# Optimization experiments

Hardware: AMD Instinct MI355X
Metric: run time of the kernel (lower is better)

The kernel has to match this reference:

```python
import jax, jax.numpy as jnp
import numpy as np

ALPHA = 1.0  # self.a buffer (alpha=1.0 default)


def setup_inputs() -> dict:
    key = jax.random.key(0)
    k1, k2, k3 = jax.random.split(key, 3)
    B, S, DIN, DOUT = 4, 2048, 4096, 4096
    # activations and weights are int8 in [-127, 127)
    x = jax.random.randint(k1, (B, S, DIN), -127, 127, dtype=jnp.int8)
    weight = jax.random.randint(k2, (DOUT, DIN), -127, 127, dtype=jnp.int8)
    bias = jax.random.normal(k3, (1, DOUT), dtype=jnp.float32)
    return {"x": x, "weight": weight, "bias": bias}


def reference(x, weight, bias):
    # x: [B, S, DIN] int8; weight: [DOUT, DIN] int8; bias: [1, DOUT] fp32
    x_shape = x.shape
    x2 = x.reshape(-1, x_shape[-1])  # [B*S, DIN]
    y = jnp.matmul(x2, weight.T, preferred_element_type=jnp.int32)  # [B*S, DOUT] int32
    # epilogue: y + round(bias / alpha); int32 + fp32 promotes to fp32 (matches torch)
    y = y.astype(jnp.float32) + jnp.round(bias / ALPHA)
    return y.reshape(*x_shape[:-1], y.shape[-1])
```

## Files before the change

### kernel.cpp

```cpp
#include <hip/hip_runtime.h>
#include <stdint.h>
#include <math.h>


typedef int i32x4 __attribute__((ext_vector_type(4)));
typedef int i32x16 __attribute__((ext_vector_type(16)));

static constexpr int Mdim = 8192;
static constexpr int Ndim = 4096;
static constexpr int Kdim = 4096;
static constexpr int BM = 128;
static constexpr int BN = 128;
static constexpr int BKb = 64;
static constexpr int NKT = Kdim / BKb;
static constexpr int BUF_BYTES = 16384;

typedef const __attribute__((address_space(1))) unsigned int gu32;
typedef __attribute__((address_space(3))) unsigned int lu32;

__device__ __forceinline__ void gload_lds16(const int8_t* g, char* l) {
    __builtin_amdgcn_global_load_lds((gu32*)g, (lu32*)l, 16, 0, 0);
}

__global__ void pack_i32_to_i8(const int* __restrict__ in,
                               unsigned int* __restrict__ out, int n4) {
    int idx = blockIdx.x * blockDim.x + threadIdx.x;
    int stride = gridDim.x * blockDim.x;
    for (int i = idx; i < n4; i += stride) {
        i32x4 v = ((const i32x4*)in)[i];
        unsigned int o = ((unsigned)v[0] & 0xffu)
                       | (((unsigned)v[1] & 0xffu) << 8)
                       | (((unsigned)v[2] & 0xffu) << 16)
                       | (((unsigned)v[3]) << 24);
        out[i] = o;
    }
}

__global__ __launch_bounds__(256, 2) void w8a8_gemm_kernel(
    const int8_t* __restrict__ X, const int8_t* __restrict__ Wt,
    const float* __restrict__ bias, float* __restrict__ out)
{
    __shared__ char smem[2 * BUF_BYTES];

    const int tid   = threadIdx.x;
    const int w     = tid >> 6;
    const int l     = tid & 63;
    const int lrow  = l & 31;
    const int khalf = l >> 5;
    const int wr    = w >> 1;
    const int wc    = w & 1;

    const int bm = blockIdx.x * BM;
    const int bn = blockIdx.y * BN;

    const int8_t* gA0 = X  + (long)(bm +      l) * Kdim + w * 16;
    const int8_t* gA1 = X  + (long)(bm + 64 + l) * Kdim + w * 16;
    const int8_t* gB0 = Wt + (long)(bn +      l) * Kdim + w * 16;
    const int8_t* gB1 = Wt + (long)(bn + 64 + l) * Kdim + w * 16;
    const int lA0 = (w * 128 +      l) * 16;
    const int lA1 = (w * 128 + 64 + l) * 16;
    const int lB0 = 8192 + (w * 128 +      l) * 16;
    const int lB1 = 8192 + (w * 128 + 64 + l) * 16;

    const int aRowOff = (wr * 64 + lrow) * 16;
    const int bRowOff = (wc * 64 + lrow) * 16;

    i32x16 acc[2][2] = {};

    gload_lds16(gA0, &smem[lA0]);
    gload_lds16(gA1, &smem[lA1]);
    gload_lds16(gB0, &smem[lB0]);
    gload_lds16(gB1, &smem[lB1]);
    asm volatile("s_waitcnt vmcnt(0)" ::: "memory");
    __syncthreads();

    int buf = 0;
    for (int kt = 0; kt < NKT; ++kt) {
        if (kt + 1 < NKT) {
            const int kb = (kt + 1) * BKb;
            const int nb = (buf ^ 1) * BUF_BYTES;
            gload_lds16(gA0 + kb, &smem[nb + lA0]);
            gload_lds16(gA1 + kb, &smem[nb + lA1]);
            gload_lds16(gB0 + kb, &smem[nb + lB0]);
            gload_lds16(gB1 + kb, &smem[nb + lB1]);
        }

        const char* sb = &smem[buf * BUF_BYTES];
        i32x4 af[2][2], bf[2][2];
#pragma unroll
        for (int ks = 0; ks < 2; ++ks) {
            const int slot = (ks * 2 + khalf) * 2048;
            af[0][ks] = *(const i32x4*)(sb + slot + aRowOff);
            af[1][ks] = *(const i32x4*)(sb + slot + aRowOff + 32 * 16);
            bf[0][ks] = *(const i32x4*)(sb + 8192 + slot + bRowOff);
            bf[1][ks] = *(const i32x4*)(sb + 8192 + slot + bRowOff + 32 * 16);
        }

#pragma unroll
        for (int ks = 0; ks < 2; ++ks)
#pragma unroll
            for (int mi = 0; mi < 2; ++mi)
#pragma unroll
                for (int ni = 0; ni < 2; ++ni)
                    acc[mi][ni] = __builtin_amdgcn_mfma_i32_32x32x32_i8(
                        af[mi][ks], bf[ni][ks], acc[mi][ni], 0, 0, 0);

        asm volatile("s_waitcnt vmcnt(0)" ::: "memory");
        __syncthreads();
        buf ^= 1;
    }

#pragma unroll
    for (int ni = 0; ni < 2; ++ni) {
        const int col = bn + wc * 64 + ni * 32 + lrow;
        const float badd = rintf(bias[col]);
#pragma unroll
        for (int mi = 0; mi < 2; ++mi) {
            const int rbase = bm + wr * 64 + mi * 32 + 4 * khalf;
#pragma unroll
            for (int r = 0; r < 16; ++r) {
                const int row = rbase + (r & 3) + 8 * (r >> 2);
                out[(long)row * Ndim + col] = (float)acc[mi][ni][r] + badd;
            }
        }
    }
}

extern "C" void kernel_launch(void* const* d_in, const int* in_sizes, int n_in,
                              void* d_out, int out_size, void* d_ws, size_t ws_size,
                              hipStream_t stream) {
    const int*   X32  = (const int*)d_in[0];
    const int*   W32  = (const int*)d_in[1];
    const float* bias = (const float*)d_in[2];
    float* out = (float*)d_out;

    int8_t* Xp = (int8_t*)d_ws;
    int8_t* Wp = (int8_t*)d_ws + (size_t)Mdim * Kdim;

    const int nX4 = Mdim * Kdim / 4;
    const int nW4 = Ndim * Kdim / 4;
    pack_i32_to_i8<<<2048, 256, 0, stream>>>(X32, (unsigned int*)Xp, nX4);
    pack_i32_to_i8<<<2048, 256, 0, stream>>>(W32, (unsigned int*)Wp, nW4);

    dim3 grid(Mdim / BM, Ndim / BN);
    w8a8_gemm_kernel<<<grid, dim3(256), 0, stream>>>(Xp, Wp, bias, out);
}
```

Before: 507.1 us.

## Switch to 256x256 tiles with 8-wave interleaved load/MFMA pipeline

Replaces the 128x128x64 four-wave GEMM with a 256x256x128 eight-wave kernel using 16x16x64 int8 MFMAs. Global-to-LDS loads for the next tiles are split into quarters and interleaved between four MFMA phases, with barriers and priority raising to overlap memory and compute. This is meant to raise arithmetic intensity and hide load latency, at the cost of much larger LDS use (one block per CU), more registers, and possible LDS bank conflicts.

```diff
diff --git a/kernel.cpp b/kernel.cpp
--- a/kernel.cpp
+++ b/kernel.cpp
@@ -4,16 +4,15 @@
 
 
 typedef int i32x4 __attribute__((ext_vector_type(4)));
-typedef int i32x16 __attribute__((ext_vector_type(16)));
 
 static constexpr int Mdim = 8192;
 static constexpr int Ndim = 4096;
 static constexpr int Kdim = 4096;
-static constexpr int BM = 128;
-static constexpr int BN = 128;
-static constexpr int BKb = 64;
+static constexpr int BM = 256;
+static constexpr int BN = 256;
+static constexpr int BKb = 128;
 static constexpr int NKT = Kdim / BKb;
-static constexpr int BUF_BYTES = 16384;
+static constexpr int BUF_BYTES = 65536;
 
 typedef const __attribute__((address_space(1))) unsigned int gu32;
 typedef __attribute__((address_space(3))) unsigned int lu32;
@@ -36,92 +35,159 @@
     }
 }
 
-__global__ __launch_bounds__(256, 2) void w8a8_gemm_kernel(
+__global__ __launch_bounds__(512, 2) void w8a8_gemm_256(
     const int8_t* __restrict__ X, const int8_t* __restrict__ Wt,
     const float* __restrict__ bias, float* __restrict__ out)
 {
     __shared__ char smem[2 * BUF_BYTES];
 
-    const int tid   = threadIdx.x;
-    const int w     = tid >> 6;
-    const int l     = tid & 63;
-    const int lrow  = l & 31;
-    const int khalf = l >> 5;
-    const int wr    = w >> 1;
-    const int wc    = w & 1;
+    const int tid = threadIdx.x;
+    const int w   = tid >> 6;
+    const int l   = tid & 63;
+    const int fr  = l & 15;
+    const int fk  = l >> 4;
+    const int wm  = w >> 2;
+    const int wn  = w & 3;
 
     const int bm = blockIdx.x * BM;
     const int bn = blockIdx.y * BN;
 
-    const int8_t* gA0 = X  + (long)(bm +      l) * Kdim + w * 16;
-    const int8_t* gA1 = X  + (long)(bm + 64 + l) * Kdim + w * 16;
-    const int8_t* gB0 = Wt + (long)(bn +      l) * Kdim + w * 16;
-    const int8_t* gB1 = Wt + (long)(bn + 64 + l) * Kdim + w * 16;
-    const int lA0 = (w * 128 +      l) * 16;
-    const int lA1 = (w * 128 + 64 + l) * 16;
-    const int lB0 = 8192 + (w * 128 +      l) * 16;
-    const int lB1 = 8192 + (w * 128 + 64 + l) * 16;
-
-    const int aRowOff = (wr * 64 + lrow) * 16;
-    const int bRowOff = (wc * 64 + lrow) * 16;
-
-    i32x16 acc[2][2] = {};
-
-    gload_lds16(gA0, &smem[lA0]);
-    gload_lds16(gA1, &smem[lA1]);
-    gload_lds16(gB0, &smem[lB0]);
-    gload_lds16(gB1, &smem[lB1]);
-    asm volatile("s_waitcnt vmcnt(0)" ::: "memory");
+    const int8_t* gA = X  + (size_t)(bm + l) * Kdim + w * 16;
+    const int8_t* gB = Wt + (size_t)(bn + l) * Kdim + w * 16;
+    const int ldsAw = w * 2048 + l * 16;
+    const int ldsBw = 32768 + w * 2048 + l * 16;
+
+    auto stageA = [&](int t, int hm) {
+        const int bufo = (t & 1) * BUF_BYTES;
+        const size_t ko = (size_t)t * BKb;
+#pragma unroll
+        for (int s = 0; s < 2; ++s)
+            gload_lds16(gA + (size_t)(hm * 128 + s * 64) * Kdim + ko,
+                        &smem[bufo + hm * 16384 + s * 1024 + ldsAw]);
+    };
+    auto stageB = [&](int t, int hn) {
+        const int bufo = (t & 1) * BUF_BYTES;
+        const size_t ko = (size_t)t * BKb;
+#pragma unroll
+        for (int s = 0; s < 2; ++s)
+            gload_lds16(gB + (size_t)(hn * 128 + s * 64) * Kdim + ko,
+                        &smem[bufo + hn * 16384 + s * 1024 + ldsBw]);
+    };
+
+    const int aBase = wm * 16384 + fk * 2048 + fr * 16;
+    const int bBase = 32768 + (wn >> 1) * 16384 + fk * 2048
+                    + ((wn & 1) * 64 + fr) * 16;
+
+    i32x4 acc[8][4] = {};
+    i32x4 a[4][2], b[4][2];
+
+    stageB(0, 0); stageB(0, 1); stageA(0, 0); stageA(0, 1);
+    stageB(1, 0); stageB(1, 1);
+    asm volatile("s_waitcnt vmcnt(4)" ::: "memory");
     __syncthreads();
 
-    int buf = 0;
-    for (int kt = 0; kt < NKT; ++kt) {
-        if (kt + 1 < NKT) {
-            const int kb = (kt + 1) * BKb;
-            const int nb = (buf ^ 1) * BUF_BYTES;
-            gload_lds16(gA0 + kb, &smem[nb + lA0]);
-            gload_lds16(gA1 + kb, &smem[nb + lA1]);
-            gload_lds16(gB0 + kb, &smem[nb + lB0]);
-            gload_lds16(gB1 + kb, &smem[nb + lB1]);
+    for (int t = 0; t < NKT; ++t) {
+        const int p = (t & 1) * BUF_BYTES;
+
+#pragma unroll
+        for (int ks = 0; ks < 2; ++ks) {
+#pragma unroll
+            for (int j = 0; j < 4; ++j)
+                a[j][ks] = *(const i32x4*)&smem[p + aBase + ks * 8192 + j * 256];
+#pragma unroll
+            for (int ni = 0; ni < 2; ++ni)
+                b[ni][ks] = *(const i32x4*)&smem[p + bBase + ks * 8192 + ni * 256];
         }
-
-        const char* sb = &smem[buf * BUF_BYTES];
-        i32x4 af[2][2], bf[2][2];
-#pragma unroll
-        for (int ks = 0; ks < 2; ++ks) {
-            const int slot = (ks * 2 + khalf) * 2048;
-            af[0][ks] = *(const i32x4*)(sb + slot + aRowOff);
-            af[1][ks] = *(const i32x4*)(sb + slot + aRowOff + 32 * 16);
-            bf[0][ks] = *(const i32x4*)(sb + 8192 + slot + bRowOff);
-            bf[1][ks] = *(const i32x4*)(sb + 8192 + slot + bRowOff + 32 * 16);
+        if (t + 1 < NKT) stageA(t + 1, 0);
+        __builtin_amdgcn_s_barrier();
+        asm volatile("s_waitcnt lgkmcnt(0)" ::: "memory");
+        __builtin_amdgcn_sched_barrier(0);
+        __builtin_amdgcn_s_setprio(1);
+#pragma unroll
+        for (int ks = 0; ks < 2; ++ks)
+#pragma unroll
+            for (int j = 0; j < 4; ++j)
+#pragma unroll
+                for (int ni = 0; ni < 2; ++ni)
+                    acc[j][ni] = __builtin_amdgcn_mfma_i32_16x16x64_i8(
+                        a[j][ks], b[ni][ks], acc[j][ni], 0, 0, 0);
+        __builtin_amdgcn_s_setprio(0);
+        __builtin_amdgcn_s_barrier();
+
+#pragma unroll
+        for (int ks = 0; ks < 2; ++ks)
+#pragma unroll
+            for (int ni = 2; ni < 4; ++ni)
+                b[ni][ks] = *(const i32x4*)&smem[p + bBase + ks * 8192 + ni * 256];
+        if (t + 1 < NKT) stageA(t + 1, 1);
+        __builtin_amdgcn_s_barrier();
+        asm volatile("s_waitcnt lgkmcnt(0)" ::: "memory");
+        __builtin_amdgcn_sched_barrier(0);
+        __builtin_amdgcn_s_setprio(1);
+#pragma unroll
+        for (int ks = 0; ks < 2; ++ks)
+#pragma unroll
+            for (int j = 0; j < 4; ++j)
+#pragma unroll
+                for (int ni = 2; ni < 4; ++ni)
+                    acc[j][ni] = __builtin_amdgcn_mfma_i32_16x16x64_i8(
+                        a[j][ks], b[ni][ks], acc[j][ni], 0, 0, 0);
+        __builtin_amdgcn_s_setprio(0);
+        __builtin_amdgcn_s_barrier();
+
+#pragma unroll
+        for (int ks = 0; ks < 2; ++ks)
+#pragma unroll
+            for (int j = 0; j < 4; ++j)
+                a[j][ks] = *(const i32x4*)&smem[p + aBase + ks * 8192 + 1024 + j * 256];
+        if (t + 2 < NKT) stageB(t + 2, 0);
+        __builtin_amdgcn_s_barrier();
+        asm volatile("s_waitcnt lgkmcnt(0)" ::: "memory");
+        __builtin_amdgcn_sched_barrier(0);
+        __builtin_amdgcn_s_setprio(1);
+#pragma unroll
+        for (int ks = 0; ks < 2; ++ks)
+#pragma unroll
+            for (int j = 0; j < 4; ++j)
+#pragma unroll
+                for (int ni = 0; ni < 2; ++ni)
+                    acc[4 + j][ni] = __builtin_amdgcn_mfma_i32_16x16x64_i8(
+                        a[j][ks], b[ni][ks], acc[4 + j][ni], 0, 0, 0);
+        __builtin_amdgcn_s_setprio(0);
+        __builtin_amdgcn_s_barrier();
+
+        if (t + 2 < NKT) stageB(t + 2, 1);
+        __builtin_amdgcn_s_barrier();
+        __builtin_amdgcn_s_setprio(1);
+#pragma unroll
+        for (int ks = 0; ks < 2; ++ks)
+#pragma unroll
+            for (int j = 0; j < 4; ++j)
+#pragma unroll
+                for (int ni = 2; ni < 4; ++ni)
+                    acc[4 + j][ni] = __builtin_amdgcn_mfma_i32_16x16x64_i8(
+                        a[j][ks], b[ni][ks], acc[4 + j][ni], 0, 0, 0);
+        __builtin_amdgcn_s_setprio(0);
+        if (t + 1 < NKT) {
+            if (t + 1 == NKT - 1) asm volatile("s_waitcnt vmcnt(0)" ::: "memory");
+            else                  asm volatile("s_waitcnt vmcnt(4)" ::: "memory");
         }
-
-#pragma unroll
-        for (int ks = 0; ks < 2; ++ks)
-#pragma unroll
-            for (int mi = 0; mi < 2; ++mi)
-#pragma unroll
-                for (int ni = 0; ni < 2; ++ni)
-                    acc[mi][ni] = __builtin_amdgcn_mfma_i32_32x32x32_i8(
-                        af[mi][ks], bf[ni][ks], acc[mi][ni], 0, 0, 0);
-
-        asm volatile("s_waitcnt vmcnt(0)" ::: "memory");
-        __syncthreads();
-        buf ^= 1;
+        __builtin_amdgcn_s_barrier();
     }
 
-#pragma unroll
-    for (int ni = 0; ni < 2; ++ni) {
-        const int col = bn + wc * 64 + ni * 32 + lrow;
-        const float badd = rintf(bias[col]);
-#pragma unroll
-        for (int mi = 0; mi < 2; ++mi) {
-            const int rbase = bm + wr * 64 + mi * 32 + 4 * khalf;
-#pragma unroll
-            for (int r = 0; r < 16; ++r) {
-                const int row = rbase + (r & 3) + 8 * (r >> 2);
-                out[(long)row * Ndim + col] = (float)acc[mi][ni][r] + badd;
-            }
+    float bv[4];
+#pragma unroll
+    for (int ni = 0; ni < 4; ++ni)
+        bv[ni] = rintf(bias[bn + wn * 64 + ni * 16 + fr]);
+#pragma unroll
+    for (int mi = 0; mi < 8; ++mi) {
+        const int rbase = bm + wm * 128 + mi * 16 + fk * 4;
+#pragma unroll
+        for (int ni = 0; ni < 4; ++ni) {
+            const int col = bn + wn * 64 + ni * 16 + fr;
+#pragma unroll
+            for (int r = 0; r < 4; ++r)
+                out[(size_t)(rbase + r) * Ndim + col] = (float)acc[mi][ni][r] + bv[ni];
         }
     }
 }
@@ -143,5 +209,5 @@
     pack_i32_to_i8<<<2048, 256, 0, stream>>>(W32, (unsigned int*)Wp, nW4);
 
     dim3 grid(Mdim / BM, Ndim / BN);
-    w8a8_gemm_kernel<<<grid, dim3(256), 0, stream>>>(Xp, Wp, bias, out);
-}
+    w8a8_gemm_256<<<grid, dim3(512), 0, stream>>>(Xp, Wp, bias, out);
+}
```

Result: faster. 411.6 us (-18.8%).
